# Optimization experiments

Hardware: AMD Instinct MI355X
Metric: run time of the kernel (lower is better)

The kernel has to match this reference:

```python
import jax, jax.numpy as jnp
import numpy as np
import math

B, L, D, H = 2, 2048, 1024, 16
HD = D // H
DILATION, WINDOW, CAUSAL = 2, 512, True
EPS = 1e-5  # nn.LayerNorm default


def _ln(x, g, b):
    mu = x.mean(-1, keepdims=True)
    var = ((x - mu) ** 2).mean(-1, keepdims=True)
    return (x - mu) * jax.lax.rsqrt(var + EPS) * g + b


def setup_inputs() -> dict:
    key = jax.random.key(0)
    ks = jax.random.split(key, 8)
    s = 0.02  # small init scale to keep activations sane
    return {
        'x': jax.random.normal(ks[0], (B, L, D), jnp.float32),
        'ln1_g': jnp.ones((D,), jnp.float32),
        'ln1_b': jnp.zeros((D,), jnp.float32),
        'Wqkv': jax.random.normal(ks[1], (D, 3 * D), jnp.float32) * s,
        'bqkv': jnp.zeros((3 * D,), jnp.float32),
        'Wout': jax.random.normal(ks[2], (D, D), jnp.float32) * s,
        'bout': jnp.zeros((D,), jnp.float32),
        'ln2_g': jnp.ones((D,), jnp.float32),
        'ln2_b': jnp.zeros((D,), jnp.float32),
        'W1': jax.random.normal(ks[3], (D, 4 * D), jnp.float32) * s,
        'b1': jnp.zeros((4 * D,), jnp.float32),
        'W2': jax.random.normal(ks[4], (4 * D, D), jnp.float32) * s,
        'b2': jnp.zeros((D,), jnp.float32),
    }


def _keep_mask():
    # True = allowed. Matches _build_dilated_keep_mask.
    idx = jnp.arange(L, dtype=jnp.int32)
    delta = idx[:, None] - idx[None, :]
    keep = (jnp.remainder(delta, DILATION) == 0)
    keep = keep & (jnp.abs(delta) <= WINDOW)
    if CAUSAL:
        keep = keep & (delta >= 0)
    return keep  # [L, L]


def reference(x, ln1_g, ln1_b, Wqkv, bqkv, Wout, bout, ln2_g, ln2_b, W1, b1, W2, b2):
    # --- attention sub-block (pre-norm) ---
    h = _ln(x, ln1_g, ln1_b)                          # [B,L,D]
    qkv = (h @ Wqkv + bqkv).reshape(B, L, 3, H, HD)
    q = qkv[:, :, 0].transpose(0, 2, 1, 3)            # [B,H,L,HD]
    k = qkv[:, :, 1].transpose(0, 2, 1, 3)
    v = qkv[:, :, 2].transpose(0, 2, 1, 3)
    scale = 1.0 / math.sqrt(HD)
    scores = jnp.einsum('bhqd,bhkd->bhqk', q, k) * scale
    keep = _keep_mask()                               # [L,L] broadcast over B,H
    scores = jnp.where(keep, scores, jnp.float32(-1e30))
    attn = jax.nn.softmax(scores, axis=-1)
    o = jnp.einsum('bhqk,bhkd->bhqd', attn, v)        # [B,H,L,HD]
    o = o.transpose(0, 2, 1, 3).reshape(B, L, D)
    x = x + (o @ Wout + bout)
    # --- FFN sub-block (pre-norm) ---
    h2 = _ln(x, ln2_g, ln2_b)
    f = jax.nn.gelu(h2 @ W1 + b1, approximate=False)  # nn.GELU default = exact
    x = x + (f @ W2 + b2)
    return x
```

## Files before the change

kernel.cpp:

```cpp
#include <hip/hip_runtime.h>

typedef unsigned short u16;
typedef short short8 __attribute__((ext_vector_type(8)));
typedef float floatx4 __attribute__((ext_vector_type(4)));

#define B_  2
#define L_  2048
#define D_  1024
#define H_  16
#define HD_ 64
#define M_  (B_*L_)
#define LP_ 1024
#define WP_ 256

__device__ __forceinline__ float b2f(u16 u) {
    union { unsigned int i; float f; } c; c.i = ((unsigned int)u) << 16; return c.f;
}
__device__ __forceinline__ u16 f2b(float f) {
    union { float f; unsigned int i; } c; c.f = f;
    unsigned int u = c.i;
    u = u + 0x7FFFu + ((u >> 16) & 1u);
    return (u16)(u >> 16);
}
__device__ __forceinline__ float ldrawf(const void* p, size_t i, bool isbf16) {
    return isbf16 ? b2f(((const u16*)p)[i]) : ((const float*)p)[i];
}
__device__ __forceinline__ u16 ldraw16(const void* p, size_t i, bool isbf16) {
    return isbf16 ? ((const u16*)p)[i] : f2b(((const float*)p)[i]);
}
__device__ __forceinline__ float gelu_f(float x) {
    float x3 = x * x * x;
    float y2 = 1.5957691216057308f * (x + 0.044715f * x3);
    float e  = __expf(y2);
    float th = 1.0f - 2.0f / (e + 1.0f);
    return 0.5f * x * (1.0f + th);
}
__device__ __forceinline__ void gload16(const u16* g, u16* l) {
    __builtin_amdgcn_global_load_lds(
        (__attribute__((address_space(1))) void*)(g),
        (__attribute__((address_space(3))) void*)(l), 16, 0, 0);
}

__global__ void probe_k(const u16* x, int* flag) {
    int t = threadIdx.x;
    unsigned int u = x[2 * t];
    unsigned int e = (u >> 7) & 0xFF;
    bool sane = (e >= 100 && e <= 140);
    unsigned long long m = __ballot(sane);
    if (t == 0) *flag = (__popcll(m) >= 32) ? 1 : 0;
}

__global__ __launch_bounds__(256) void transpose_k(const void* __restrict__ in,
                                                   u16* __restrict__ out, int K, int N,
                                                   const int* flagp) {
    bool isb = (*flagp != 0);
    __shared__ u16 tile[32][33];
    int tx = threadIdx.x & 31;
    int ty = threadIdx.x >> 5;
    int nb = blockIdx.x * 32;
    int kb = blockIdx.y * 32;
    #pragma unroll
    for (int j = 0; j < 32; j += 8)
        tile[ty + j][tx] = ldraw16(in, (size_t)(kb + ty + j) * N + nb + tx, isb);
    __syncthreads();
    #pragma unroll
    for (int j = 0; j < 32; j += 8)
        out[(size_t)(nb + ty + j) * K + kb + tx] = tile[tx][ty + j];
}

template<int SRC>
__global__ __launch_bounds__(256) void ln_k(const void* __restrict__ x, const void* __restrict__ g,
                                            const void* __restrict__ bb, u16* __restrict__ out,
                                            const int* flagp) {
    bool isb = (*flagp != 0);
    int row = blockIdx.x;
    int t = threadIdx.x;
    float v[4]; float s = 0.f, s2 = 0.f;
    #pragma unroll
    for (int i = 0; i < 4; i++) {
        size_t idx = (size_t)row * D_ + t + 256 * i;
        float f = (SRC == 1) ? ((const float*)x)[idx] : ldrawf(x, idx, isb);
        v[i] = f; s += f; s2 += f * f;
    }
    #pragma unroll
    for (int off = 32; off >= 1; off >>= 1) { s += __shfl_xor(s, off); s2 += __shfl_xor(s2, off); }
    __shared__ float red[8];
    int wave = t >> 6;
    if ((t & 63) == 0) { red[wave] = s; red[4 + wave] = s2; }
    __syncthreads();
    s  = red[0] + red[1] + red[2] + red[3];
    s2 = red[4] + red[5] + red[6] + red[7];
    float mu  = s * (1.0f / 1024.0f);
    float var = s2 * (1.0f / 1024.0f) - mu * mu;
    float rs  = rsqrtf(var + 1e-5f);
    #pragma unroll
    for (int i = 0; i < 4; i++) {
        int c = t + 256 * i;
        out[(size_t)row * D_ + c] = f2b((v[i] - mu) * rs * ldrawf(g, c, isb) + ldrawf(bb, c, isb));
    }
}

template<int NT, int OUT, int RES, int GELU, int SPLITK>
__global__ __launch_bounds__(256) void gemm128_k(const u16* __restrict__ A,
                                                 const u16* __restrict__ BT,
                                                 const void* __restrict__ bias,
                                                 const void* __restrict__ resid,
                                                 void* __restrict__ C,
                                                 int M, int N, int K,
                                                 const int* flagp) {
    constexpr int TN = NT * 32;
    __shared__ __align__(16) u16 a_s[2][128 * 32];
    __shared__ __align__(16) u16 b_s[2][TN * 32];
    bool isb = (*flagp != 0);

    const int bm = blockIdx.y, bn = blockIdx.x;
    const int kz = (SPLITK > 1) ? blockIdx.z : 0;
    const int Kc = K / SPLITK;
    const int k_beg = kz * Kc;
    const int nIter = Kc / 32;

    const int t = threadIdx.x, w = t >> 6, lane = t & 63;
    const int wm = w >> 1, wn = w & 1;
    const int quad = lane >> 4, r16 = lane & 15;

    const int lr  = lane >> 2;
    const int lcg = (((lane & 3) ^ ((lr >> 1) & 3))) * 8;
    const u16* Ag0 = A  + (size_t)(bm * 128 + w * 32 + lr) * K + lcg + k_beg;
    const u16* Ag1 = Ag0 + (size_t)16 * K;
    const u16* Bg0 = BT + (size_t)(bn * TN + w * (TN / 4) + lr) * K + lcg + k_beg;
    const u16* Bg1 = Bg0 + (size_t)16 * K;
    const int aoff0 = (w * 32 + lr) * 32 + (lane & 3) * 8;
    const int aoff1 = aoff0 + 16 * 32;
    const int boff0 = (w * (TN / 4) + lr) * 32 + (lane & 3) * 8;
    const int boff1 = boff0 + 16 * 32;

    const int sw = ((r16 >> 1) & 3);
    floatx4 acc[4][NT] = {};

    gload16(Ag0, a_s[0] + aoff0);
    gload16(Ag1, a_s[0] + aoff1);
    gload16(Bg0, b_s[0] + boff0);
    if constexpr (NT == 4) gload16(Bg1, b_s[0] + boff1);

    for (int i = 0; i < nIter; i++) {
        const int cur = i & 1, nxt = cur ^ 1;
        __syncthreads();
        if (i + 1 < nIter) {
            int kc2 = (i + 1) * 32;
            gload16(Ag0 + kc2, a_s[nxt] + aoff0);
            gload16(Ag1 + kc2, a_s[nxt] + aoff1);
            gload16(Bg0 + kc2, b_s[nxt] + boff0);
            if constexpr (NT == 4) gload16(Bg1 + kc2, b_s[nxt] + boff1);
        }
        short8 af[4], bf[NT];
        #pragma unroll
        for (int mt = 0; mt < 4; mt++)
            af[mt] = *(const short8*)(a_s[cur] + (wm * 64 + mt * 16 + r16) * 32 + (quad ^ sw) * 8);
        #pragma unroll
        for (int nt = 0; nt < NT; nt++)
            bf[nt] = *(const short8*)(b_s[cur] + (wn * (TN / 2) + nt * 16 + r16) * 32 + (quad ^ sw) * 8);
        #pragma unroll
        for (int mt = 0; mt < 4; mt++)
            #pragma unroll
            for (int nt = 0; nt < NT; nt++)
                acc[mt][nt] = __builtin_amdgcn_mfma_f32_16x16x32_bf16(af[mt], bf[nt], acc[mt][nt], 0, 0, 0);
    }

    #pragma unroll
    for (int mt = 0; mt < 4; mt++)
      #pragma unroll
      for (int nt = 0; nt < NT; nt++)
        #pragma unroll
        for (int r = 0; r < 4; r++) {
            int row = bm * 128 + wm * 64 + mt * 16 + quad * 4 + r;
            int col = bn * TN + wn * (TN / 2) + nt * 16 + r16;
            size_t oi = (size_t)row * N + col;
            if (OUT == 3) {
                ((u16*)C)[(size_t)kz * M * N + oi] = f2b(acc[mt][nt][r]);
                continue;
            }
            float v = acc[mt][nt][r] + ldrawf(bias, col, isb);
            if (GELU) v = gelu_f(v);
            if (RES == 1) v += ldrawf(resid, (size_t)row * N + col, isb);
            if (RES == 2) v += ((const float*)resid)[(size_t)row * N + col];
            if (OUT == 0) ((float*)C)[oi] = v;
            else if (OUT == 1) ((u16*)C)[oi] = f2b(v);
            else {
                if (isb) ((u16*)C)[oi] = f2b(v);
                else     ((float*)C)[oi] = v;
            }
        }
}

__global__ __launch_bounds__(256) void reduce_k(const u16* __restrict__ part,
                                                const float* __restrict__ x1,
                                                const void* __restrict__ b2,
                                                void* __restrict__ out,
                                                const int* flagp) {
    bool isb = (*flagp != 0);
    size_t i0 = ((size_t)blockIdx.x * 256 + threadIdx.x) * 4;
    float4 xv = *(const float4*)(x1 + i0);
    float r[4] = { xv.x, xv.y, xv.z, xv.w };
    #pragma unroll
    for (int j = 0; j < 4; j++) r[j] += ldrawf(b2, (i0 + j) & (D_ - 1), isb);
    #pragma unroll
    for (int z = 0; z < 4; z++) {
        ushort4 pv = *(const ushort4*)(part + (size_t)z * M_ * D_ + i0);
        r[0] += b2f(pv.x); r[1] += b2f(pv.y); r[2] += b2f(pv.z); r[3] += b2f(pv.w);
    }
    if (isb) {
        ushort4 ov = { f2b(r[0]), f2b(r[1]), f2b(r[2]), f2b(r[3]) };
        *(ushort4*)((u16*)out + i0) = ov;
    } else {
        float4 ov = { r[0], r[1], r[2], r[3] };
        *(float4*)((float*)out + i0) = ov;
    }
}

__global__ __launch_bounds__(256) void repack_k(const u16* __restrict__ qkv,
                                                u16* __restrict__ Qp, u16* __restrict__ Kp,
                                                u16* __restrict__ Vt) {
    int pid = blockIdx.x;
    int lt  = blockIdx.y;
    int b = pid >> 5, p = (pid >> 4) & 1, h = pid & 15;
    int t = threadIdx.x;
    int srow = t >> 2;
    int scol = (t & 3) * 16;

    int lp = lt * 64 + srow;
    int l  = 2 * lp + p;
    const u16* src = qkv + ((size_t)b * L_ + l) * (3 * D_) + h * HD_;
    size_t dst = ((size_t)pid * LP_ + lp) * HD_;

    *(int4*)(Qp + dst + scol)     = *(const int4*)(src + scol);
    *(int4*)(Qp + dst + scol + 8) = *(const int4*)(src + scol + 8);
    *(int4*)(Kp + dst + scol)     = *(const int4*)(src + D_ + scol);
    *(int4*)(Kp + dst + scol + 8) = *(const int4*)(src + D_ + scol + 8);

    __shared__ u16 vt[64][72];
    *(int4*)(&vt[srow][scol])     = *(const int4*)(src + 2 * D_ + scol);
    *(int4*)(&vt[srow][scol + 8]) = *(const int4*)(src + 2 * D_ + scol + 8);
    __syncthreads();
    union { u16 s[16]; int4 v[2]; } tmp;
    #pragma unroll
    for (int jj = 0; jj < 16; jj++) tmp.s[jj] = vt[scol + jj][srow];
    u16* vdst = Vt + ((size_t)pid * HD_ + srow) * LP_ + lt * 64 + scol;
    *(int4*)(vdst)     = tmp.v[0];
    *(int4*)(vdst + 8) = tmp.v[1];
}

#define FS 72
__global__ __launch_bounds__(256) void fattn_k(const u16* __restrict__ Qp,
                                               const u16* __restrict__ Kp,
                                               const u16* __restrict__ Vt,
                                               u16* __restrict__ o) {
    __shared__ __align__(16) u16 Qs[64 * FS];
    __shared__ __align__(16) u16 Ks[64 * FS];
    __shared__ __align__(16) u16 Vs[64 * FS];
    __shared__ __align__(16) u16 Ps[4][16 * FS];

    const int pid = blockIdx.x, qt = blockIdx.y;
    const int b = pid >> 5, p = (pid >> 4) & 1, h = pid & 15;
    const int t = threadIdx.x, w = t >> 6, lane = t & 63;
    const int quad = lane >> 4, r16 = lane & 15;
    const int q0 = qt * 64;

    const int srow = t >> 2;
    const int scol = (t & 3) * 16;

    const u16* qsrc = Qp + ((size_t)pid * LP_ + q0 + srow) * HD_;
    *(int4*)(Qs + srow * FS + scol)     = *(const int4*)(qsrc + scol);
    *(int4*)(Qs + srow * FS + scol + 8) = *(const int4*)(qsrc + scol + 8);
    __syncthreads();

    const short8 qf0 = *(const short8*)(Qs + (w * 16 + r16) * FS + quad * 8);
    const short8 qf1 = *(const short8*)(Qs + (w * 16 + r16) * FS + quad * 8 + 32);

    floatx4 oacc[4] = {};
    float mrow[4] = {-INFINITY, -INFINITY, -INFINITY, -INFINITY};
    float lrow[4] = {};

    const int kt0 = (qt >= 4) ? qt - 4 : 0;
    const int qrow_base = q0 + w * 16 + quad * 4;

    for (int kt = kt0; kt <= qt; ++kt) {
        __syncthreads();
        const u16* ksrc = Kp + ((size_t)pid * LP_ + kt * 64 + srow) * HD_;
        *(int4*)(Ks + srow * FS + scol)     = *(const int4*)(ksrc + scol);
        *(int4*)(Ks + srow * FS + scol + 8) = *(const int4*)(ksrc + scol + 8);
        const u16* vsrc = Vt + ((size_t)pid * HD_ + srow) * LP_ + kt * 64;
        *(int4*)(Vs + srow * FS + scol)     = *(const int4*)(vsrc + scol);
        *(int4*)(Vs + srow * FS + scol + 8) = *(const int4*)(vsrc + scol + 8);
        __syncthreads();

        floatx4 s4[4];
        #pragma unroll
        for (int nt = 0; nt < 4; nt++) {
            short8 kf0 = *(const short8*)(Ks + (nt * 16 + r16) * FS + quad * 8);
            short8 kf1 = *(const short8*)(Ks + (nt * 16 + r16) * FS + quad * 8 + 32);
            floatx4 z = {};
            z = __builtin_amdgcn_mfma_f32_16x16x32_bf16(qf0, kf0, z, 0, 0, 0);
            z = __builtin_amdgcn_mfma_f32_16x16x32_bf16(qf1, kf1, z, 0, 0, 0);
            s4[nt] = z;
        }

        float sv[4][4];
        #pragma unroll
        for (int nt = 0; nt < 4; nt++) {
            int kcol = kt * 64 + nt * 16 + r16;
            #pragma unroll
            for (int r = 0; r < 4; r++) {
                int kq = kcol - (qrow_base + r);
                bool valid = (kq <= 0) && (kq >= -WP_);
                sv[nt][r] = valid ? s4[nt][r] * 0.125f : -1e30f;
            }
        }

        float mx[4];
        #pragma unroll
        for (int r = 0; r < 4; r++)
            mx[r] = fmaxf(fmaxf(sv[0][r], sv[1][r]), fmaxf(sv[2][r], sv[3][r]));
        #pragma unroll
        for (int off = 8; off >= 1; off >>= 1)
            #pragma unroll
            for (int r = 0; r < 4; r++) mx[r] = fmaxf(mx[r], __shfl_xor(mx[r], off));

        float al[4];
        #pragma unroll
        for (int r = 0; r < 4; r++) {
            float mnew = fmaxf(mrow[r], mx[r]);
            al[r] = __expf(mrow[r] - mnew);
            mrow[r] = mnew;
        }

        float ps[4][4], rs[4] = {};
        #pragma unroll
        for (int nt = 0; nt < 4; nt++)
            #pragma unroll
            for (int r = 0; r < 4; r++) {
                float pv = __expf(sv[nt][r] - mrow[r]);
                ps[nt][r] = pv; rs[r] += pv;
            }
        #pragma unroll
        for (int off = 8; off >= 1; off >>= 1)
            #pragma unroll
            for (int r = 0; r < 4; r++) rs[r] += __shfl_xor(rs[r], off);
        #pragma unroll
        for (int r = 0; r < 4; r++) lrow[r] = lrow[r] * al[r] + rs[r];
        #pragma unroll
        for (int nt = 0; nt < 4; nt++)
            #pragma unroll
            for (int r = 0; r < 4; r++) oacc[nt][r] *= al[r];

        #pragma unroll
        for (int nt = 0; nt < 4; nt++)
            #pragma unroll
            for (int r = 0; r < 4; r++)
                Ps[w][(quad * 4 + r) * FS + nt * 16 + r16] = f2b(ps[nt][r]);
        short8 pf0 = *(const short8*)(&Ps[w][r16 * FS + quad * 8]);
        short8 pf1 = *(const short8*)(&Ps[w][r16 * FS + quad * 8 + 32]);

        #pragma unroll
        for (int nt = 0; nt < 4; nt++) {
            short8 vf0 = *(const short8*)(Vs + (nt * 16 + r16) * FS + quad * 8);
            short8 vf1 = *(const short8*)(Vs + (nt * 16 + r16) * FS + quad * 8 + 32);
            oacc[nt] = __builtin_amdgcn_mfma_f32_16x16x32_bf16(pf0, vf0, oacc[nt], 0, 0, 0);
            oacc[nt] = __builtin_amdgcn_mfma_f32_16x16x32_bf16(pf1, vf1, oacc[nt], 0, 0, 0);
        }
    }

    float inv[4];
    #pragma unroll
    for (int r = 0; r < 4; r++) inv[r] = 1.0f / lrow[r];
    #pragma unroll
    for (int nt = 0; nt < 4; nt++)
        #pragma unroll
        for (int r = 0; r < 4; r++) {
            int qp = qrow_base + r;
            int l  = 2 * qp + p;
            int d  = nt * 16 + r16;
            o[((size_t)b * L_ + l) * D_ + h * HD_ + d] = f2b(oacc[nt][r] * inv[r]);
        }
}

extern "C" void kernel_launch(void* const* d_in, const int* in_sizes, int n_in,
                              void* d_out, int out_size, void* d_ws, size_t ws_size,
                              hipStream_t stream) {
    (void)in_sizes; (void)n_in; (void)out_size; (void)ws_size;
    const void* x     = d_in[0];
    const void* ln1_g = d_in[1];
    const void* ln1_b = d_in[2];
    const void* Wqkv  = d_in[3];
    const void* bqkv  = d_in[4];
    const void* Wout  = d_in[5];
    const void* bout  = d_in[6];
    const void* ln2_g = d_in[7];
    const void* ln2_b = d_in[8];
    const void* W1    = d_in[9];
    const void* b1    = d_in[10];
    const void* W2    = d_in[11];
    const void* b2    = d_in[12];

    char* ws = (char*)d_ws;
    const size_t MB = 1024 * 1024;
    u16*   wqkvT = (u16*)ws;
    u16*   qkv   = (u16*)(ws + 6  * MB);
    u16*   woutT = (u16*)(ws + 30 * MB);
    u16*   fbuf  = (u16*)ws;
    u16*   w1T   = (u16*)(ws + 32 * MB);
    u16*   w2T   = (u16*)(ws + 40 * MB);
    u16*   bufA  = (u16*)(ws + 48 * MB);
    float* x1    = (float*)(ws + 56 * MB);
    u16*   Qp    = (u16*)(ws + 72 * MB);
    u16*   Kp    = (u16*)(ws + 80 * MB);
    u16*   Vt    = (u16*)(ws + 88 * MB);
    u16*   part  = (u16*)(ws + 96 * MB);
    int*   flag  = (int*)(ws + 128 * MB);

    dim3 tb(256);
    probe_k<<<1, 64, 0, stream>>>((const u16*)x, flag);

    transpose_k<<<dim3(3 * D_ / 32, D_ / 32), tb, 0, stream>>>(Wqkv, wqkvT, D_, 3 * D_, flag);
    transpose_k<<<dim3(D_ / 32, D_ / 32), tb, 0, stream>>>(Wout, woutT, D_, D_, flag);
    transpose_k<<<dim3(4 * D_ / 32, D_ / 32), tb, 0, stream>>>(W1, w1T, D_, 4 * D_, flag);
    transpose_k<<<dim3(D_ / 32, 4 * D_ / 32), tb, 0, stream>>>(W2, w2T, 4 * D_, D_, flag);

    ln_k<0><<<M_, tb, 0, stream>>>(x, ln1_g, ln1_b, bufA, flag);

    gemm128_k<4, 1, 0, 0, 1><<<dim3(3 * D_ / 128, M_ / 128), tb, 0, stream>>>(bufA, wqkvT, bqkv, nullptr, qkv, M_, 3 * D_, D_, flag);

    repack_k<<<dim3(64, 16), tb, 0, stream>>>(qkv, Qp, Kp, Vt);
    fattn_k<<<dim3(64, 16), tb, 0, stream>>>(Qp, Kp, Vt, bufA);

    gemm128_k<2, 0, 1, 0, 1><<<dim3(D_ / 64, M_ / 128), tb, 0, stream>>>(bufA, woutT, bout, x, x1, M_, D_, D_, flag);

    ln_k<1><<<M_, tb, 0, stream>>>(x1, ln2_g, ln2_b, bufA, flag);

    gemm128_k<4, 1, 0, 1, 1><<<dim3(4 * D_ / 128, M_ / 128), tb, 0, stream>>>(bufA, w1T, b1, nullptr, fbuf, M_, 4 * D_, D_, flag);

    gemm128_k<2, 3, 0, 0, 4><<<dim3(D_ / 64, M_ / 128, 4), tb, 0, stream>>>(fbuf, w2T, nullptr, nullptr, part, M_, D_, 4 * D_, flag);
    reduce_k<<<(M_ * D_) / 1024, tb, 0, stream>>>(part, x1, b2, d_out, flag);
}
```

Baseline: 401.0 us.

## Merge weight transposes, add 2-wave GEMM, drop Q/K repack, prefetch attention tiles

Fuses the four weight-transpose launches into one kernel. Adds a 128-thread, 2-wave GEMM with a 128x128 tile and larger per-wave accumulators, used for the QKV and FFN-up projections. The attention kernel now reads Q and K straight from the qkv buffer, so only V is repacked, and it register-prefetches the next K/V tile while computing the current one. The aims are fewer launches, less intermediate memory traffic and better latency hiding. The costs are strided Q/K reads and higher register pressure in the new GEMM.

```diff
diff --git a/kernel.cpp b/kernel.cpp
--- a/kernel.cpp
+++ b/kernel.cpp
@@ -50,15 +50,12 @@
     if (t == 0) *flag = (__popcll(m) >= 32) ? 1 : 0;
 }
 
-__global__ __launch_bounds__(256) void transpose_k(const void* __restrict__ in,
-                                                   u16* __restrict__ out, int K, int N,
-                                                   const int* flagp) {
-    bool isb = (*flagp != 0);
+__device__ __forceinline__ void tr_body(const void* in, u16* out, int K, int N,
+                                        int bx, int by, bool isb) {
     __shared__ u16 tile[32][33];
     int tx = threadIdx.x & 31;
     int ty = threadIdx.x >> 5;
-    int nb = blockIdx.x * 32;
-    int kb = blockIdx.y * 32;
+    int nb = bx * 32, kb = by * 32;
     #pragma unroll
     for (int j = 0; j < 32; j += 8)
         tile[ty + j][tx] = ldraw16(in, (size_t)(kb + ty + j) * N + nb + tx, isb);
@@ -66,6 +63,16 @@
     #pragma unroll
     for (int j = 0; j < 32; j += 8)
         out[(size_t)(nb + ty + j) * K + kb + tx] = tile[tx][ty + j];
+}
+__global__ __launch_bounds__(256) void transpose_all_k(
+        const void* w0, const void* w1, const void* w2, const void* w3,
+        u16* o0, u16* o1, u16* o2, u16* o3, const int* flagp) {
+    bool isb = (*flagp != 0);
+    int id = blockIdx.x;
+    if (id < 3072)            { int l = id;         tr_body(w0, o0, 1024, 3072, l % 96,  l / 96,  isb); }
+    else if (id < 4096)       { int l = id - 3072;  tr_body(w1, o1, 1024, 1024, l % 32,  l / 32,  isb); }
+    else if (id < 8192)       { int l = id - 4096;  tr_body(w2, o2, 1024, 4096, l % 128, l / 128, isb); }
+    else                      { int l = id - 8192;  tr_body(w3, o3, 4096, 1024, l % 32,  l / 32,  isb); }
 }
 
 template<int SRC>
@@ -100,7 +107,78 @@
     }
 }
 
-template<int NT, int OUT, int RES, int GELU, int SPLITK>
+template<int GELU>
+__global__ __launch_bounds__(128) void gemm2w_k(const u16* __restrict__ A,
+                                                const u16* __restrict__ BT,
+                                                const void* __restrict__ bias,
+                                                u16* __restrict__ C,
+                                                int M, int N, int K,
+                                                const int* flagp) {
+    __shared__ __align__(16) u16 a_s[2][128 * 32];
+    __shared__ __align__(16) u16 b_s[2][128 * 32];
+    bool isb = (*flagp != 0);
+
+    const int bm = blockIdx.y, bn = blockIdx.x;
+    const int t = threadIdx.x, w = t >> 6, lane = t & 63;
+    const int quad = lane >> 4, r16 = lane & 15;
+    const int nIter = K / 32;
+
+    const int lr  = lane >> 2;
+    const int lcg = (((lane & 3) ^ ((lr >> 1) & 3))) * 8;
+    const u16* Ag[4]; const u16* Bg[4]; int aloff[4], bloff[4];
+    #pragma unroll
+    for (int j = 0; j < 4; j++) {
+        Ag[j] = A  + (size_t)(bm * 128 + w * 64 + j * 16 + lr) * K + lcg;
+        Bg[j] = BT + (size_t)(bn * 128 + w * 64 + j * 16 + lr) * K + lcg;
+        aloff[j] = (w * 64 + j * 16 + lr) * 32 + (lane & 3) * 8;
+        bloff[j] = aloff[j];
+    }
+    const int sw = ((r16 >> 1) & 3);
+    floatx4 acc[4][8] = {};
+
+    #pragma unroll
+    for (int j = 0; j < 4; j++) { gload16(Ag[j], a_s[0] + aloff[j]); gload16(Bg[j], b_s[0] + bloff[j]); }
+
+    for (int i = 0; i < nIter; i++) {
+        const int cur = i & 1, nxt = cur ^ 1;
+        __syncthreads();
+        if (i + 1 < nIter) {
+            int kc = (i + 1) * 32;
+            #pragma unroll
+            for (int j = 0; j < 4; j++) {
+                gload16(Ag[j] + kc, a_s[nxt] + aloff[j]);
+                gload16(Bg[j] + kc, b_s[nxt] + bloff[j]);
+            }
+        }
+        short8 af[4], bf[8];
+        #pragma unroll
+        for (int mt = 0; mt < 4; mt++)
+            af[mt] = *(const short8*)(a_s[cur] + (w * 64 + mt * 16 + r16) * 32 + (quad ^ sw) * 8);
+        #pragma unroll
+        for (int nt = 0; nt < 8; nt++)
+            bf[nt] = *(const short8*)(b_s[cur] + (nt * 16 + r16) * 32 + (quad ^ sw) * 8);
+        #pragma unroll
+        for (int mt = 0; mt < 4; mt++)
+            #pragma unroll
+            for (int nt = 0; nt < 8; nt++)
+                acc[mt][nt] = __builtin_amdgcn_mfma_f32_16x16x32_bf16(af[mt], bf[nt], acc[mt][nt], 0, 0, 0);
+    }
+
+    #pragma unroll
+    for (int mt = 0; mt < 4; mt++)
+      #pragma unroll
+      for (int nt = 0; nt < 8; nt++)
+        #pragma unroll
+        for (int r = 0; r < 4; r++) {
+            int row = bm * 128 + w * 64 + mt * 16 + quad * 4 + r;
+            int col = bn * 128 + nt * 16 + r16;
+            float v = acc[mt][nt][r] + ldrawf(bias, col, isb);
+            if (GELU) v = gelu_f(v);
+            C[(size_t)row * N + col] = f2b(v);
+        }
+}
+
+template<int NT, int OUT, int RES, int SPLITK>
 __global__ __launch_bounds__(256) void gemm128_k(const u16* __restrict__ A,
                                                  const u16* __restrict__ BT,
                                                  const void* __restrict__ bias,
@@ -177,17 +255,10 @@
             size_t oi = (size_t)row * N + col;
             if (OUT == 3) {
                 ((u16*)C)[(size_t)kz * M * N + oi] = f2b(acc[mt][nt][r]);
-                continue;
-            }
-            float v = acc[mt][nt][r] + ldrawf(bias, col, isb);
-            if (GELU) v = gelu_f(v);
-            if (RES == 1) v += ldrawf(resid, (size_t)row * N + col, isb);
-            if (RES == 2) v += ((const float*)resid)[(size_t)row * N + col];
-            if (OUT == 0) ((float*)C)[oi] = v;
-            else if (OUT == 1) ((u16*)C)[oi] = f2b(v);
-            else {
-                if (isb) ((u16*)C)[oi] = f2b(v);
-                else     ((float*)C)[oi] = v;
+            } else {
+                float v = acc[mt][nt][r] + ldrawf(bias, col, isb);
+                if (RES == 1) v += ldrawf(resid, (size_t)row * N + col, isb);
+                ((float*)C)[oi] = v;
             }
         }
 }
@@ -217,9 +288,8 @@
     }
 }
 
-__global__ __launch_bounds__(256) void repack_k(const u16* __restrict__ qkv,
-                                                u16* __restrict__ Qp, u16* __restrict__ Kp,
-                                                u16* __restrict__ Vt) {
+__global__ __launch_bounds__(256) void repack_v_k(const u16* __restrict__ qkv,
+                                                  u16* __restrict__ Vt) {
     int pid = blockIdx.x;
     int lt  = blockIdx.y;
     int b = pid >> 5, p = (pid >> 4) & 1, h = pid & 15;
@@ -229,17 +299,11 @@
 
     int lp = lt * 64 + srow;
     int l  = 2 * lp + p;
-    const u16* src = qkv + ((size_t)b * L_ + l) * (3 * D_) + h * HD_;
-    size_t dst = ((size_t)pid * LP_ + lp) * HD_;
-
-    *(int4*)(Qp + dst + scol)     = *(const int4*)(src + scol);
-    *(int4*)(Qp + dst + scol + 8) = *(const int4*)(src + scol + 8);
-    *(int4*)(Kp + dst + scol)     = *(const int4*)(src + D_ + scol);
-    *(int4*)(Kp + dst + scol + 8) = *(const int4*)(src + D_ + scol + 8);
+    const u16* src = qkv + ((size_t)b * L_ + l) * (3 * D_) + 2 * D_ + h * HD_;
 
     __shared__ u16 vt[64][72];
-    *(int4*)(&vt[srow][scol])     = *(const int4*)(src + 2 * D_ + scol);
-    *(int4*)(&vt[srow][scol + 8]) = *(const int4*)(src + 2 * D_ + scol + 8);
+    *(int4*)(&vt[srow][scol])     = *(const int4*)(src + scol);
+    *(int4*)(&vt[srow][scol + 8]) = *(const int4*)(src + scol + 8);
     __syncthreads();
     union { u16 s[16]; int4 v[2]; } tmp;
     #pragma unroll
@@ -250,8 +314,7 @@
 }
 
 #define FS 72
-__global__ __launch_bounds__(256) void fattn_k(const u16* __restrict__ Qp,
-                                               const u16* __restrict__ Kp,
+__global__ __launch_bounds__(256) void fattn_k(const u16* __restrict__ qkv,
                                                const u16* __restrict__ Vt,
                                                u16* __restrict__ o) {
     __shared__ __align__(16) u16 Qs[64 * FS];
@@ -268,7 +331,7 @@
     const int srow = t >> 2;
     const int scol = (t & 3) * 16;
 
-    const u16* qsrc = Qp + ((size_t)pid * LP_ + q0 + srow) * HD_;
+    const u16* qsrc = qkv + ((size_t)b * L_ + 2 * (q0 + srow) + p) * (3 * D_) + h * HD_;
     *(int4*)(Qs + srow * FS + scol)     = *(const int4*)(qsrc + scol);
     *(int4*)(Qs + srow * FS + scol + 8) = *(const int4*)(qsrc + scol + 8);
     __syncthreads();
@@ -283,15 +346,30 @@
     const int kt0 = (qt >= 4) ? qt - 4 : 0;
     const int qrow_base = q0 + w * 16 + quad * 4;
 
+    auto kaddr = [&](int kt) {
+        return qkv + ((size_t)b * L_ + 2 * (kt * 64 + srow) + p) * (3 * D_) + D_ + h * HD_;
+    };
+    auto vaddr = [&](int kt) {
+        return Vt + ((size_t)pid * HD_ + srow) * LP_ + kt * 64;
+    };
+    int4 kr0 = *(const int4*)(kaddr(kt0) + scol);
+    int4 kr1 = *(const int4*)(kaddr(kt0) + scol + 8);
+    int4 vr0 = *(const int4*)(vaddr(kt0) + scol);
+    int4 vr1 = *(const int4*)(vaddr(kt0) + scol + 8);
+
     for (int kt = kt0; kt <= qt; ++kt) {
         __syncthreads();
-        const u16* ksrc = Kp + ((size_t)pid * LP_ + kt * 64 + srow) * HD_;
-        *(int4*)(Ks + srow * FS + scol)     = *(const int4*)(ksrc + scol);
-        *(int4*)(Ks + srow * FS + scol + 8) = *(const int4*)(ksrc + scol + 8);
-        const u16* vsrc = Vt + ((size_t)pid * HD_ + srow) * LP_ + kt * 64;
-        *(int4*)(Vs + srow * FS + scol)     = *(const int4*)(vsrc + scol);
-        *(int4*)(Vs + srow * FS + scol + 8) = *(const int4*)(vsrc + scol + 8);
+        *(int4*)(Ks + srow * FS + scol)     = kr0;
+        *(int4*)(Ks + srow * FS + scol + 8) = kr1;
+        *(int4*)(Vs + srow * FS + scol)     = vr0;
+        *(int4*)(Vs + srow * FS + scol + 8) = vr1;
         __syncthreads();
+        if (kt < qt) {
+            kr0 = *(const int4*)(kaddr(kt + 1) + scol);
+            kr1 = *(const int4*)(kaddr(kt + 1) + scol + 8);
+            vr0 = *(const int4*)(vaddr(kt + 1) + scol);
+            vr1 = *(const int4*)(vaddr(kt + 1) + scol + 8);
+        }
 
         floatx4 s4[4];
         #pragma unroll
@@ -411,33 +489,28 @@
     u16*   w2T   = (u16*)(ws + 40 * MB);
     u16*   bufA  = (u16*)(ws + 48 * MB);
     float* x1    = (float*)(ws + 56 * MB);
-    u16*   Qp    = (u16*)(ws + 72 * MB);
-    u16*   Kp    = (u16*)(ws + 80 * MB);
-    u16*   Vt    = (u16*)(ws + 88 * MB);
-    u16*   part  = (u16*)(ws + 96 * MB);
-    int*   flag  = (int*)(ws + 128 * MB);
+    u16*   Vt    = (u16*)(ws + 72 * MB);
+    u16*   part  = (u16*)(ws + 80 * MB);
+    int*   flag  = (int*)(ws + 112 * MB);
 
     dim3 tb(256);
     probe_k<<<1, 64, 0, stream>>>((const u16*)x, flag);
 
-    transpose_k<<<dim3(3 * D_ / 32, D_ / 32), tb, 0, stream>>>(Wqkv, wqkvT, D_, 3 * D_, flag);
-    transpose_k<<<dim3(D_ / 32, D_ / 32), tb, 0, stream>>>(Wout, woutT, D_, D_, flag);
-    transpose_k<<<dim3(4 * D_ / 32, D_ / 32), tb, 0, stream>>>(W1, w1T, D_, 4 * D_, flag);
-    transpose_k<<<dim3(D_ / 32, 4 * D_ / 32), tb, 0, stream>>>(W2, w2T, 4 * D_, D_, flag);
+    transpose_all_k<<<12288, tb, 0, stream>>>(Wqkv, Wout, W1, W2, wqkvT, woutT, w1T, w2T, flag);
 
     ln_k<0><<<M_, tb, 0, stream>>>(x, ln1_g, ln1_b, bufA, flag);
 
-    gemm128_k<4, 1, 0, 0, 1><<<dim3(3 * D_ / 128, M_ / 128), tb, 0, stream>>>(bufA, wqkvT, bqkv, nullptr, qkv, M_, 3 * D_, D_, flag);
-
-    repack_k<<<dim3(64, 16), tb, 0, stream>>>(qkv, Qp, Kp, Vt);
-    fattn_k<<<dim3(64, 16), tb, 0, stream>>>(Qp, Kp, Vt, bufA);
-
-    gemm128_k<2, 0, 1, 0, 1><<<dim3(D_ / 64, M_ / 128), tb, 0, stream>>>(bufA, woutT, bout, x, x1, M_, D_, D_, flag);
+    gemm2w_k<0><<<dim3(3 * D_ / 128, M_ / 128), dim3(128), 0, stream>>>(bufA, wqkvT, bqkv, qkv, M_, 3 * D_, D_, flag);
+
+    repack_v_k<<<dim3(64, 16), tb, 0, stream>>>(qkv, Vt);
+    fattn_k<<<dim3(64, 16), tb, 0, stream>>>(qkv, Vt, bufA);
+
+    gemm128_k<2, 0, 1, 1><<<dim3(D_ / 64, M_ / 128), tb, 0, stream>>>(bufA, woutT, bout, x, x1, M_, D_, D_, flag);
 
     ln_k<1><<<M_, tb, 0, stream>>>(x1, ln2_g, ln2_b, bufA, flag);
 
-    gemm128_k<4, 1, 0, 1, 1><<<dim3(4 * D_ / 128, M_ / 128), tb, 0, stream>>>(bufA, w1T, b1, nullptr, fbuf, M_, 4 * D_, D_, flag);
-
-    gemm128_k<2, 3, 0, 0, 4><<<dim3(D_ / 64, M_ / 128, 4), tb, 0, stream>>>(fbuf, w2T, nullptr, nullptr, part, M_, D_, 4 * D_, flag);
+    gemm2w_k<1><<<dim3(4 * D_ / 128, M_ / 128), dim3(128), 0, stream>>>(bufA, w1T, b1, fbuf, M_, 4 * D_, D_, flag);
+
+    gemm128_k<2, 3, 0, 4><<<dim3(D_ / 64, M_ / 128, 4), tb, 0, stream>>>(fbuf, w2T, nullptr, nullptr, part, M_, D_, 4 * D_, flag);
     reduce_k<<<(M_ * D_) / 1024, tb, 0, stream>>>(part, x1, b2, d_out, flag);
 }
```

Measured after the change: 466.4 us. +16.3%, slower.
